# Optimization experiments

Hardware: AMD Instinct MI355X
Metric: run time of the kernel (lower is better)

Reference implementation:

```python
import jax, jax.numpy as jnp
import numpy as np

DIM = 1024; H = 16; KVH = 4; HD = 64          # head_dim = DIM // H
I = 2048                                       # intermediate_size = 2*DIM
N = 16                                         # ssm_state_size
DTR = 64                                       # dt_rank = DIM // 16
K = 4                                          # conv kernel
BASE = 10000.0
EPS = 1.1920929e-07                            # torch F.rms_norm default eps (fp32 finfo eps)

def rms_norm(x):
    return x * jax.lax.rsqrt(jnp.mean(x * x, axis=-1, keepdims=True) + EPS)

def rope_tables(S, dims):
    inv = 1.0 / BASE ** (jnp.arange(0, dims, 2, dtype=jnp.float32) / dims)
    f = jnp.outer(jnp.arange(S, dtype=jnp.float32), inv)   # [S, dims//2]
    return jnp.cos(f), jnp.sin(f)

def apply_rope(x, cos, sin):
    half = x.shape[-1] // 2
    x1, x2 = x[..., :half], x[..., half:]
    return jnp.concatenate([x1 * cos + x2 * sin, -x1 * sin + x2 * cos], axis=-1)

def setup_inputs() -> dict:
    key = jax.random.key(0)
    ks = jax.random.split(key, 12)
    B, S = 2, 2048
    def w(k, shape, s=0.02):
        return jax.random.normal(k, shape, jnp.float32) * s
    return {
        "x": jax.random.normal(ks[0], (B, S, DIM), jnp.float32),
        "W_mamba": w(ks[1], (2 * I, DIM)),
        "W_q": w(ks[2], (DIM, DIM)),
        "W_kv": w(ks[3], (2 * KVH * HD, DIM)),
        "q_gain": jnp.full((H,), 1.0, jnp.float32),
        "conv_w": w(ks[4], (I, K), 0.2),
        "conv_b": jnp.zeros((I,), jnp.float32),
        "W_xproj": w(ks[5], (DTR + 2 * N, I)),
        "W_dt": w(ks[6], (I, DTR)),
        "b_dt": w(ks[7], (I,), 0.5),
        "A_log": jnp.log(jnp.broadcast_to(jnp.arange(1, N + 1, dtype=jnp.float32), (I, N))),
        "D": jnp.ones((I,), jnp.float32),
        "W_mamba_out": w(ks[8], (DIM, I)),
        "W_proj": w(ks[9], (DIM, DIM)),
        "merge_alpha": jnp.zeros((1,), jnp.float32),
    }

def reference(x, W_mamba, W_q, W_kv, q_gain, conv_w, conv_b, W_xproj, W_dt, b_dt,
              A_log, D, W_mamba_out, W_proj, merge_alpha):
    B, S, _ = x.shape
    # --- parallel input projection for the mamba branch ---
    mp = x @ W_mamba.T                         # [B,S,2I]
    x_ssm, gate = mp[..., :I], mp[..., I:]
    # --- attention branch (GQA + full RoPE + per-head q gain) ---
    q = (x @ W_q.T).reshape(B, S, H, HD).transpose(0, 2, 1, 3)
    kv = x @ W_kv.T
    k = kv[..., :KVH * HD].reshape(B, S, KVH, HD).transpose(0, 2, 1, 3)
    v = kv[..., KVH * HD:].reshape(B, S, KVH, HD).transpose(0, 2, 1, 3)
    q = rms_norm(q); k = rms_norm(k)
    cos, sin = rope_tables(S, HD)
    q = apply_rope(q, cos, sin)
    k = apply_rope(k, cos, sin)
    q = q * q_gain[None, :, None, None]
    nrep = H // KVH
    k = jnp.repeat(k, nrep, axis=1)
    v = jnp.repeat(v, nrep, axis=1)
    scores = jnp.einsum('bhqd,bhkd->bhqk', q, k) / jnp.sqrt(jnp.float32(HD))
    mask = jnp.tril(jnp.ones((S, S), bool))
    scores = jnp.where(mask, scores, -jnp.inf)
    y = jnp.einsum('bhqk,bhkd->bhqd', jax.nn.softmax(scores, axis=-1), v)
    attn_out = y.transpose(0, 2, 1, 3).reshape(B, S, DIM)
    # --- mamba/SSM branch: causal depthwise conv1d + silu ---
    xc = x_ssm.transpose(0, 2, 1)              # [B,I,S]
    u = jax.lax.conv_general_dilated(xc, conv_w[:, None, :], (1,), [(K - 1, 0)],
                                     dimension_numbers=('NCH', 'OIH', 'NCH'),
                                     feature_group_count=I) + conv_b[None, :, None]
    u = u * jax.nn.sigmoid(u)                  # silu, [B,I,S]
    u_bsi = u.transpose(0, 2, 1)               # [B,S,I]
    params = u_bsi @ W_xproj.T                 # [B,S,DTR+2N]
    dt_low = params[..., :DTR]
    Bm = params[..., DTR:DTR + N]
    Cm = params[..., DTR + N:]
    delta = jax.nn.softplus(dt_low @ W_dt.T + b_dt)   # [B,S,I] (delta_bias + softplus)
    A = -jnp.exp(A_log)                        # [I,N]
    def step(state, inp):
        d_t, b_t, c_t, u_t = inp               # [B,I],[B,N],[B,N],[B,I]
        dA = jnp.exp(d_t[:, :, None] * A[None])
        state = state * dA + d_t[:, :, None] * b_t[:, None, :] * u_t[:, :, None]
        y_t = jnp.sum(state * c_t[:, None, :], axis=-1)
        return state, y_t
    xs = (delta.transpose(1, 0, 2), Bm.transpose(1, 0, 2),
          Cm.transpose(1, 0, 2), u_bsi.transpose(1, 0, 2))
    state0 = jnp.zeros((B, I, N), x.dtype)
    _, ys = jax.lax.scan(step, state0, xs)     # ys: [S,B,I]
    y_ssm = ys.transpose(1, 0, 2) + u_bsi * D  # + D skip
    y_ssm = y_ssm * (gate * jax.nn.sigmoid(gate))      # gated by silu(z)
    mamba_out = y_ssm @ W_mamba_out.T          # [B,S,DIM]
    # --- gated merge + output projection ---
    alpha = jax.nn.sigmoid(merge_alpha)
    merged = alpha * attn_out + (1.0 - alpha) * mamba_out
    return merged @ W_proj.T
```

## Files before the change

kernel.cpp:

```cpp
#include <hip/hip_runtime.h>
#include <hip/hip_bf16.h>

#define B_   2
#define S_   2048
#define T_   4096
#define DIM_ 1024
#define H_   16
#define KVH_ 4
#define HD_  64
#define I_   2048
#define N_   16
#define DTR_ 64
#define MB   ((size_t)1 << 20)

typedef __hip_bfloat16 bf16;
typedef __attribute__((ext_vector_type(8))) short short8;
typedef __attribute__((ext_vector_type(4))) short short4v;
typedef __attribute__((ext_vector_type(4))) float f32x4;

__device__ __forceinline__ float b2f(bf16 v){ return __bfloat162float(v); }
__device__ __forceinline__ bf16  f2b(float v){ return __float2bfloat16(v); }
__device__ __forceinline__ float s2f(short s){
  return __builtin_bit_cast(float, ((unsigned int)(unsigned short)s) << 16);
}
__device__ __forceinline__ short f2s(float v){
  return (short)__builtin_bit_cast(unsigned short, f2b(v));
}

__device__ __forceinline__ void async16(const void* g, void* l) {
  __builtin_amdgcn_global_load_lds((__attribute__((address_space(1))) void*)g,
                                   (__attribute__((address_space(3))) void*)l, 16, 0, 0);
}

__global__ __launch_bounds__(256)
void cast_f2b(const float* __restrict__ in, bf16* __restrict__ out, int n4)
{
  const int i = blockIdx.x * 256 + threadIdx.x;
  if (i >= n4) return;
  const float4 v = ((const float4*)in)[i];
  short4v o;
  o.x = f2s(v.x); o.y = f2s(v.y); o.z = f2s(v.z); o.w = f2s(v.w);
  *(short4v*)(out + (size_t)i * 4) = o;
}

template<int MODE, int TS>
__global__ __launch_bounds__(256)
void gemm_nt(const bf16* __restrict__ A, int lda,
             const bf16* __restrict__ W, int ldw,
             void* __restrict__ C, int ldc,
             bf16* __restrict__ Ct, int ldt,
             const float* __restrict__ bias,
             int M, int N, int K)
{
  __shared__ __align__(16) bf16 As[128*32];
  __shared__ __align__(16) bf16 Bs[128*32];
  const int tid  = threadIdx.x;
  const int lane = tid & 63;
  const int wave = tid >> 6;
  const int l16  = lane & 15;
  const int quad = lane >> 4;
  const int wm   = (wave >> 1) << 6;
  const int wn   = (wave & 1) << 6;
  const int m0   = blockIdx.x << 7;
  const int n0   = blockIdx.y << 7;

  f32x4 acc[4][4];
  const f32x4 zero = {0.f, 0.f, 0.f, 0.f};
  #pragma unroll
  for (int i = 0; i < 4; i++)
    #pragma unroll
    for (int j = 0; j < 4; j++) acc[i][j] = zero;

  for (int k0 = 0; k0 < K; k0 += 32) {
    #pragma unroll
    for (int p = 0; p < 2; p++) {
      const int linear = ((p << 8) + tid) << 4;
      const int row    = linear >> 6;
      const int inrow  = linear & 63;
      async16(A + (size_t)(m0 + row) * lda + k0 + (inrow >> 1), (char*)As + linear);
      int wr = n0 + row; if (wr > N - 1) wr = N - 1;
      async16(W + (size_t)wr * ldw + k0 + (inrow >> 1), (char*)Bs + linear);
    }
    __syncthreads();
    short8 af[4], bfr[4];
    #pragma unroll
    for (int mt = 0; mt < 4; mt++)
      af[mt] = *(const short8*)((const char*)As + ((wm + (mt << 4) + l16) << 6) + (quad << 4));
    #pragma unroll
    for (int nt = 0; nt < 4; nt++)
      bfr[nt] = *(const short8*)((const char*)Bs + ((wn + (nt << 4) + l16) << 6) + (quad << 4));
    #pragma unroll
    for (int mt = 0; mt < 4; mt++)
      #pragma unroll
      for (int nt = 0; nt < 4; nt++)
        acc[mt][nt] = __builtin_amdgcn_mfma_f32_16x16x32_bf16(af[mt], bfr[nt], acc[mt][nt], 0, 0, 0);
    __syncthreads();
  }

  #pragma unroll
  for (int mt = 0; mt < 4; mt++) {
    #pragma unroll
    for (int nt = 0; nt < 4; nt++) {
      const int col = n0 + wn + (nt << 4) + l16;
      if (col >= N) continue;
      const int rowbase = m0 + wm + (mt << 4) + (quad << 2);
      float v[4];
      #pragma unroll
      for (int r = 0; r < 4; r++) {
        float t = acc[mt][nt][r];
        if (MODE == 2) {
          t += bias[col];
          t = (t > 20.f) ? t : log1pf(__expf(t));
        }
        v[r] = t;
      }
      if (TS == 0 || TS == 2) {
        #pragma unroll
        for (int r = 0; r < 4; r++) {
          if (MODE == 0) ((float*)C)[(size_t)(rowbase + r) * ldc + col] = v[r];
          else           ((bf16*)C)[(size_t)(rowbase + r) * ldc + col] = f2b(v[r]);
        }
      }
      if (TS >= 1) {
        short4v p;
        #pragma unroll
        for (int r = 0; r < 4; r++) p[r] = f2s(v[r]);
        *(short4v*)(Ct + (size_t)col * ldt + rowbase) = p;
      }
    }
  }
}

__global__ __launch_bounds__(256)
void qkv_prep(const bf16* __restrict__ qraw, const bf16* __restrict__ kvraw,
              const float* __restrict__ q_gain,
              bf16* __restrict__ qn, bf16* __restrict__ kn, bf16* __restrict__ vt)
{
  const int wid  = blockIdx.x * 4 + (threadIdx.x >> 6);
  const int lane = threadIdx.x & 63;
  const int t    = wid / 24;
  const int slot = wid % 24;
  const int b = t >> 11, s = t & 2047;

  float val;
  if (slot < 16)       val = b2f(qraw [(size_t)t * 1024 + slot * 64 + lane]);
  else if (slot < 20)  val = b2f(kvraw[(size_t)t * 512  + (slot - 16) * 64 + lane]);
  else                 val = b2f(kvraw[(size_t)t * 512  + 256 + (slot - 20) * 64 + lane]);

  if (slot < 20) {
    float ss = val * val;
    #pragma unroll
    for (int off = 32; off; off >>= 1) ss += __shfl_xor(ss, off);
    val *= rsqrtf(ss * (1.0f / 64.0f) + 1.1920929e-07f);
    const int j = lane & 31;
    const float x1 = __shfl(val, j);
    const float x2 = __shfl(val, j + 32);
    const float inv = powf(10000.0f, -(float)j * (1.0f / 32.0f));
    const float ang = (float)s * inv;
    const float c = cosf(ang), sn = sinf(ang);
    val = (lane < 32) ? (x1 * c + x2 * sn) : (x2 * c - x1 * sn);
  }
  if (slot < 16) {
    val *= q_gain[slot];
    qn[((size_t)(b * 16 + slot) * 2048 + s) * 64 + lane] = f2b(val);
  } else if (slot < 20) {
    kn[((size_t)(b * 4 + (slot - 16)) * 2048 + s) * 64 + lane] = f2b(val);
  } else {
    vt[((size_t)(b * 4 + (slot - 20)) * 64 + lane) * 2048 + s] = f2b(val);
  }
}

__global__ __launch_bounds__(256)
void attn_fwd(const bf16* __restrict__ qn, const bf16* __restrict__ kn,
              const bf16* __restrict__ vt, bf16* __restrict__ attn)
{
  __shared__ __align__(16) bf16 Plds[4][16][32];
  const int b = blockIdx.z, h = blockIdx.y, q0 = blockIdx.x * 64;
  const int wave = threadIdx.x >> 6, lane = threadIdx.x & 63;
  const int l16 = lane & 15, quad = lane >> 4;
  const int kvh = h >> 2;
  const bf16* Q  = qn + (size_t)(b * 16 + h)   * 2048 * 64;
  const bf16* Kp = kn + (size_t)(b * 4 + kvh)  * 2048 * 64;
  const bf16* Vt = vt + (size_t)(b * 4 + kvh)  * 64 * 2048;

  const int qrow_l = q0 + wave * 16 + l16;
  const short8 qf0 = *(const short8*)(Q + (size_t)qrow_l * 64 + quad * 8);
  const short8 qf1 = *(const short8*)(Q + (size_t)qrow_l * 64 + 32 + quad * 8);

  f32x4 acc[4];
  const f32x4 zero = {0.f, 0.f, 0.f, 0.f};
  #pragma unroll
  for (int i = 0; i < 4; i++) acc[i] = zero;
  float m_r[4], l_r[4];
  #pragma unroll
  for (int r = 0; r < 4; r++) { m_r[r] = -1e30f; l_r[r] = 0.f; }

  const int nkt = (q0 + 64) >> 5;
  for (int kt = 0; kt < nkt; kt++) {
    const int kb = kt << 5;
    const short8 kfA0 = *(const short8*)(Kp + (size_t)(kb + l16) * 64 + quad * 8);
    const short8 kfA1 = *(const short8*)(Kp + (size_t)(kb + l16) * 64 + 32 + quad * 8);
    const short8 kfB0 = *(const short8*)(Kp + (size_t)(kb + 16 + l16) * 64 + quad * 8);
    const short8 kfB1 = *(const short8*)(Kp + (size_t)(kb + 16 + l16) * 64 + 32 + quad * 8);
    f32x4 sA = zero, sB = zero;
    sA = __builtin_amdgcn_mfma_f32_16x16x32_bf16(qf0, kfA0, sA, 0, 0, 0);
    sA = __builtin_amdgcn_mfma_f32_16x16x32_bf16(qf1, kfA1, sA, 0, 0, 0);
    sB = __builtin_amdgcn_mfma_f32_16x16x32_bf16(qf0, kfB0, sB, 0, 0, 0);
    sB = __builtin_amdgcn_mfma_f32_16x16x32_bf16(qf1, kfB1, sB, 0, 0, 0);

    const int colA = kb + l16, colB = kb + 16 + l16;
    float pA[4], pB[4], alpha[4];
    #pragma unroll
    for (int r = 0; r < 4; r++) {
      const int row = q0 + wave * 16 + quad * 4 + r;
      float a  = sA[r] * 0.125f;
      float bb = sB[r] * 0.125f;
      if (colA > row) a  = -1e30f;
      if (colB > row) bb = -1e30f;
      float tm = fmaxf(a, bb);
      #pragma unroll
      for (int off = 8; off; off >>= 1) tm = fmaxf(tm, __shfl_xor(tm, off));
      const float nm = fmaxf(m_r[r], tm);
      alpha[r] = __expf(m_r[r] - nm);
      m_r[r] = nm;
      const float pa = __expf(a - nm), pb = __expf(bb - nm);
      pA[r] = pa; pB[r] = pb;
      float ps = pa + pb;
      #pragma unroll
      for (int off = 8; off; off >>= 1) ps += __shfl_xor(ps, off);
      l_r[r] = l_r[r] * alpha[r] + ps;
    }
    #pragma unroll
    for (int nt = 0; nt < 4; nt++)
      #pragma unroll
      for (int r = 0; r < 4; r++) acc[nt][r] *= alpha[r];

    __syncthreads();
    #pragma unroll
    for (int r = 0; r < 4; r++) {
      Plds[wave][quad * 4 + r][l16]      = f2b(pA[r]);
      Plds[wave][quad * 4 + r][16 + l16] = f2b(pB[r]);
    }
    __syncthreads();
    const short8 pf = *(const short8*)(&Plds[wave][l16][quad * 8]);
    #pragma unroll
    for (int nt = 0; nt < 4; nt++) {
      const short8 vf = *(const short8*)(Vt + (size_t)(nt * 16 + l16) * 2048 + kb + quad * 8);
      acc[nt] = __builtin_amdgcn_mfma_f32_16x16x32_bf16(pf, vf, acc[nt], 0, 0, 0);
    }
  }

  #pragma unroll
  for (int nt = 0; nt < 4; nt++)
    #pragma unroll
    for (int r = 0; r < 4; r++) {
      const int row = q0 + wave * 16 + quad * 4 + r;
      attn[((size_t)b * 2048 + row) * 1024 + h * 64 + nt * 16 + l16] = f2b(acc[nt][r] / l_r[r]);
    }
}

__global__ __launch_bounds__(256)
void conv_silu_t(const bf16* __restrict__ xssmT, const float* __restrict__ cw,
                 const float* __restrict__ cb, bf16* __restrict__ uT)
{
  const int i = blockIdx.x;
  const int t = blockIdx.y * 256 + threadIdx.x;
  const int s = t & 2047;
  float acc = cb[i];
  #pragma unroll
  for (int kk = 0; kk < 4; kk++) {
    if (s - 3 + kk >= 0)
      acc += s2f(__builtin_bit_cast(short, xssmT[(size_t)i * 4096 + t - 3 + kk])) * cw[i * 4 + kk];
  }
  const float sig = 1.f / (1.f + __expf(-acc));
  uT[(size_t)i * 4096 + t] = f2b(acc * sig);
}

__global__ __launch_bounds__(256)
void transpose_bf16(const bf16* __restrict__ in, bf16* __restrict__ out,
                    int R, int C)
{
  __shared__ bf16 tile[64][65];
  const int c0 = blockIdx.x * 64, r0 = blockIdx.y * 64;
  #pragma unroll
  for (int it = 0; it < 2; it++) {
    const int linear = (it * 256 + threadIdx.x) * 8;
    const int r = linear >> 6, cc = linear & 63;
    const short8 v = *(const short8*)(in + (size_t)(r0 + r) * C + c0 + cc);
    #pragma unroll
    for (int k = 0; k < 8; k++)
      tile[r][cc + k] = __builtin_bit_cast(bf16, (unsigned short)v[k]);
  }
  __syncthreads();
  #pragma unroll
  for (int it = 0; it < 2; it++) {
    const int linear = (it * 256 + threadIdx.x) * 8;
    const int oc = linear >> 6, k = linear & 63;
    short8 v;
    #pragma unroll
    for (int kk = 0; kk < 8; kk++)
      v[kk] = (short)__builtin_bit_cast(unsigned short, tile[k + kk][oc]);
    *(short8*)(out + (size_t)(c0 + oc) * R + r0 + k) = v;
  }
}

__global__ __launch_bounds__(256)
void finish_y(const bf16* __restrict__ yT, const bf16* __restrict__ gT,
              bf16* __restrict__ out)
{
  __shared__ bf16 tile[64][65];
  const int t0 = blockIdx.x * 64, i0 = blockIdx.y * 64;
  #pragma unroll
  for (int it = 0; it < 2; it++) {
    const int linear = (it * 256 + threadIdx.x) * 8;
    const int r = linear >> 6, cc = linear & 63;
    const size_t off = (size_t)(i0 + r) * 4096 + t0 + cc;
    const short8 y8 = *(const short8*)(yT + off);
    const short8 g8 = *(const short8*)(gT + off);
    #pragma unroll
    for (int k = 0; k < 8; k++) {
      const float g  = s2f(g8[k]);
      const float gs = g / (1.f + __expf(-g));
      tile[r][cc + k] = f2b(s2f(y8[k]) * gs);
    }
  }
  __syncthreads();
  #pragma unroll
  for (int it = 0; it < 2; it++) {
    const int linear = (it * 256 + threadIdx.x) * 8;
    const int oc = linear >> 6, k = linear & 63;
    short8 v;
    #pragma unroll
    for (int kk = 0; kk < 8; kk++)
      v[kk] = (short)__builtin_bit_cast(unsigned short, tile[k + kk][oc]);
    *(short8*)(out + (size_t)(t0 + oc) * 2048 + i0 + k) = v;
  }
}

__global__ __launch_bounds__(256)
void ssm_scan(const bf16* __restrict__ dltT, const bf16* __restrict__ uT,
              const bf16* __restrict__ prmT, const float* __restrict__ A_log,
              const float* __restrict__ Dv, bf16* __restrict__ youtT)
{
  __shared__ float Pl[16][17], Fl[16][17], Il[16][17];
  const int blk = blockIdx.x;
  const int b = blk >> 11, i = blk & 2047;
  const int n = threadIdx.x & 15, c = threadIdx.x >> 4;
  const float a  = -__expf(A_log[i * 16 + n]);
  const float Di = Dv[i];
  const size_t rowoff = (size_t)b * 2048 + c * 128;
  const bf16* dp = dltT  + (size_t)i * 4096 + rowoff;
  const bf16* up = uT    + (size_t)i * 4096 + rowoff;
  const bf16* Bp = prmT  + (size_t)(64 + n) * 4096 + rowoff;
  const bf16* Cp = prmT  + (size_t)(80 + n) * 4096 + rowoff;
  bf16*       yp = youtT + (size_t)i * 4096 + rowoff;

  float P = 1.f, F = 0.f;
  for (int j0 = 0; j0 < 128; j0 += 8) {
    const short8 d8 = *(const short8*)(dp + j0);
    const short8 u8 = *(const short8*)(up + j0);
    const short8 B8 = *(const short8*)(Bp + j0);
    #pragma unroll
    for (int j = 0; j < 8; j++) {
      const float dt = s2f(d8[j]);
      const float dA = __expf(dt * a);
      P *= dA;
      F = F * dA + dt * s2f(u8[j]) * s2f(B8[j]);
    }
  }
  Pl[n][c] = P; Fl[n][c] = F;
  __syncthreads();

  if (threadIdx.x < 16) {
    const int nn = threadIdx.x;
    float s = 0.f;
    #pragma unroll
    for (int cc = 0; cc < 16; cc++) {
      Il[nn][cc] = s;
      s = Fl[nn][cc] + Pl[nn][cc] * s;
    }
  }
  __syncthreads();

  float state = Il[n][c];
  for (int j0 = 0; j0 < 128; j0 += 8) {
    const short8 d8 = *(const short8*)(dp + j0);
    const short8 u8 = *(const short8*)(up + j0);
    const short8 B8 = *(const short8*)(Bp + j0);
    const short8 C8 = *(const short8*)(Cp + j0);
    short8 o8;
    #pragma unroll
    for (int j = 0; j < 8; j++) {
      const float dt = s2f(d8[j]);
      const float ut = s2f(u8[j]);
      const float dA = __expf(dt * a);
      state = state * dA + dt * ut * s2f(B8[j]);
      float y = state * s2f(C8[j]);
      y += __shfl_xor(y, 1); y += __shfl_xor(y, 2);
      y += __shfl_xor(y, 4); y += __shfl_xor(y, 8);
      o8[j] = f2s(y + ut * Di);
    }
    if (n == 0) *(short8*)(yp + j0) = o8;
  }
}

__global__ __launch_bounds__(256)
void merge_k(const bf16* __restrict__ attn, const bf16* __restrict__ mamba,
             const float* __restrict__ malpha, bf16* __restrict__ merged)
{
  const size_t idx = (size_t)blockIdx.x * 256 + threadIdx.x;
  const float al = 1.f / (1.f + __expf(-malpha[0]));
  merged[idx] = f2b(al * b2f(attn[idx]) + (1.f - al) * b2f(mamba[idx]));
}

extern "C" void kernel_launch(void* const* d_in, const int* in_sizes, int n_in,
                              void* d_out, int out_size, void* d_ws, size_t ws_size,
                              hipStream_t stream)
{
  const float* x_f     = (const float*)d_in[0];
  const float* Wm_f    = (const float*)d_in[1];
  const float* Wq_f    = (const float*)d_in[2];
  const float* Wkv_f   = (const float*)d_in[3];
  const float* q_gain  = (const float*)d_in[4];
  const float* conv_w  = (const float*)d_in[5];
  const float* conv_b  = (const float*)d_in[6];
  const float* Wxp_f   = (const float*)d_in[7];
  const float* Wdt_f   = (const float*)d_in[8];
  const float* b_dt    = (const float*)d_in[9];
  const float* A_log   = (const float*)d_in[10];
  const float* Dv      = (const float*)d_in[11];
  const float* Wmo_f   = (const float*)d_in[12];
  const float* Wp_f    = (const float*)d_in[13];
  const float* malpha  = (const float*)d_in[14];

  char* wp = (char*)d_ws;
  bf16*  xb    = (bf16*)(wp + 0 * MB);
  bf16*  Wm_b  = (bf16*)(wp + 8 * MB);
  bf16*  Wq_b  = (bf16*)(wp + 16 * MB);
  bf16*  Wkv_b = (bf16*)(wp + 18 * MB);
  bf16*  xssmT = (bf16*)(wp + 19 * MB);
  bf16*  gateT = (bf16*)(wp + 35 * MB);
  bf16*  u     = (bf16*)(wp + 51 * MB);
  bf16*  uT    = (bf16*)(wp + 67 * MB);
  bf16*  qraw  = (bf16*)(wp + 83 * MB);
  bf16*  kvraw = (bf16*)(wp + 91 * MB);
  bf16*  dltT  = (bf16*)(wp + 95 * MB);
  bf16*  qn    = (bf16*)(wp + 0 * MB);
  bf16*  kn    = (bf16*)(wp + 8 * MB);
  bf16*  vtb   = (bf16*)(wp + 10 * MB);
  bf16*  Wxp_b = (bf16*)(wp + 12 * MB);
  bf16*  Wdt_b = (bf16*)(wp + 12 * MB + 512 * 1024);
  bf16*  prm   = (bf16*)(wp + 13 * MB);
  bf16*  prmT  = (bf16*)(wp + 13 * MB + 768 * 1024);
  bf16*  Wp_b  = (bf16*)(wp + 16 * MB);
  bf16*  attnb = (bf16*)(wp + 83 * MB);
  bf16*  Wmo_b = (bf16*)(wp + 91 * MB);
  bf16*  ybuf  = (bf16*)(wp + 19 * MB);
  bf16*  ybufT = (bf16*)(wp + 51 * MB);
  bf16*  mam   = (bf16*)(wp + 35 * MB);
  bf16*  mrg   = (bf16*)(wp + 43 * MB);
  (void)ws_size; (void)in_sizes; (void)n_in; (void)out_size;

  auto cast = [&](const float* src, bf16* dst, int n) {
    const int n4 = n >> 2;
    cast_f2b<<<dim3((n4 + 255) / 256), 256, 0, stream>>>(src, dst, n4);
  };
  cast(x_f,   xb,    T_ * 1024);
  cast(Wm_f,  Wm_b,  4096 * 1024);
  cast(Wq_f,  Wq_b,  1024 * 1024);
  cast(Wkv_f, Wkv_b, 512 * 1024);

  gemm_nt<1,1><<<dim3(32, 16), 256, 0, stream>>>(xb, 1024, Wm_b,               1024, nullptr, 0, xssmT, 4096, nullptr, T_, 2048, 1024);
  gemm_nt<1,1><<<dim3(32, 16), 256, 0, stream>>>(xb, 1024, Wm_b + 2048 * 1024, 1024, nullptr, 0, gateT, 4096, nullptr, T_, 2048, 1024);
  gemm_nt<1,0><<<dim3(32, 8),  256, 0, stream>>>(xb, 1024, Wq_b,  1024, qraw,  1024, nullptr, 0, nullptr, T_, 1024, 1024);
  gemm_nt<1,0><<<dim3(32, 4),  256, 0, stream>>>(xb, 1024, Wkv_b, 1024, kvraw,  512, nullptr, 0, nullptr, T_,  512, 1024);

  qkv_prep<<<dim3((T_ * 24) / 4), 256, 0, stream>>>(qraw, kvraw, q_gain, qn, kn, vtb);
  conv_silu_t<<<dim3(2048, 16), 256, 0, stream>>>(xssmT, conv_w, conv_b, uT);
  attn_fwd<<<dim3(32, 16, 2), 256, 0, stream>>>(qn, kn, vtb, attnb);
  transpose_bf16<<<dim3(64, 32), 256, 0, stream>>>(uT, u, 2048, 4096);

  cast(Wxp_f, Wxp_b, 96 * 2048);
  cast(Wdt_f, Wdt_b, 2048 * 64);
  cast(Wmo_f, Wmo_b, 1024 * 2048);
  cast(Wp_f,  Wp_b,  1024 * 1024);

  gemm_nt<1,2><<<dim3(32, 1),  256, 0, stream>>>(u, 2048, Wxp_b, 2048, prm, 96, prmT, 4096, nullptr, T_, 96, 2048);
  gemm_nt<2,1><<<dim3(32, 16), 256, 0, stream>>>(prm, 96, Wdt_b, 64, nullptr, 0, dltT, 4096, b_dt, T_, 2048, 64);
  ssm_scan<<<dim3(4096), 256, 0, stream>>>(dltT, uT, prmT, A_log, Dv, ybufT);
  finish_y<<<dim3(64, 32), 256, 0, stream>>>(ybufT, gateT, ybuf);
  gemm_nt<1,0><<<dim3(32, 8),  256, 0, stream>>>(ybuf, 2048, Wmo_b, 2048, mam, 1024, nullptr, 0, nullptr, T_, 1024, 2048);

  merge_k<<<dim3(16384), 256, 0, stream>>>(attnb, mam, malpha, mrg);
  gemm_nt<0,0><<<dim3(32, 8),  256, 0, stream>>>(mrg, 1024, Wp_b, 1024, (float*)d_out, 1024, nullptr, 0, nullptr, T_, 1024, 1024);
}
```

Measured before the change: 903.9 us.

## Widen attention key tile, bound loop per wave, drop block barriers

The causal attention loop now processes 64 keys per iteration instead of 32, and each wave stops at its own 16-row causal bound rather than the whole block's bound. The two __syncthreads around the per-wave P staging buffer are removed, since each wave only touches its own LDS slice. That slice is padded to a stride of 80 to reduce bank conflicts. The aim is to cut barrier stalls, loop overhead and wasted masked work, at the cost of more registers for the wider score tile.

```diff
diff --git a/kernel.cpp b/kernel.cpp
--- a/kernel.cpp
+++ b/kernel.cpp
@@ -174,18 +174,18 @@
 void attn_fwd(const bf16* __restrict__ qn, const bf16* __restrict__ kn,
               const bf16* __restrict__ vt, bf16* __restrict__ attn)
 {
-  __shared__ __align__(16) bf16 Plds[4][16][32];
-  const int b = blockIdx.z, h = blockIdx.y, q0 = blockIdx.x * 64;
+  __shared__ __align__(16) bf16 Plds[4][16][80];
+  const int b = blockIdx.z, h = blockIdx.y;
   const int wave = threadIdx.x >> 6, lane = threadIdx.x & 63;
   const int l16 = lane & 15, quad = lane >> 4;
+  const int q0 = blockIdx.x * 64 + wave * 16;
   const int kvh = h >> 2;
-  const bf16* Q  = qn + (size_t)(b * 16 + h)   * 2048 * 64;
-  const bf16* Kp = kn + (size_t)(b * 4 + kvh)  * 2048 * 64;
-  const bf16* Vt = vt + (size_t)(b * 4 + kvh)  * 64 * 2048;
-
-  const int qrow_l = q0 + wave * 16 + l16;
-  const short8 qf0 = *(const short8*)(Q + (size_t)qrow_l * 64 + quad * 8);
-  const short8 qf1 = *(const short8*)(Q + (size_t)qrow_l * 64 + 32 + quad * 8);
+  const bf16* Q  = qn + (size_t)(b * 16 + h)  * 2048 * 64;
+  const bf16* Kp = kn + (size_t)(b * 4 + kvh) * 2048 * 64;
+  const bf16* Vt = vt + (size_t)(b * 4 + kvh) * 64 * 2048;
+
+  const short8 qf0 = *(const short8*)(Q + (size_t)(q0 + l16) * 64 + quad * 8);
+  const short8 qf1 = *(const short8*)(Q + (size_t)(q0 + l16) * 64 + 32 + quad * 8);
 
   f32x4 acc[4];
   const f32x4 zero = {0.f, 0.f, 0.f, 0.f};
@@ -195,39 +195,41 @@
   #pragma unroll
   for (int r = 0; r < 4; r++) { m_r[r] = -1e30f; l_r[r] = 0.f; }
 
-  const int nkt = (q0 + 64) >> 5;
-  for (int kt = 0; kt < nkt; kt++) {
-    const int kb = kt << 5;
-    const short8 kfA0 = *(const short8*)(Kp + (size_t)(kb + l16) * 64 + quad * 8);
-    const short8 kfA1 = *(const short8*)(Kp + (size_t)(kb + l16) * 64 + 32 + quad * 8);
-    const short8 kfB0 = *(const short8*)(Kp + (size_t)(kb + 16 + l16) * 64 + quad * 8);
-    const short8 kfB1 = *(const short8*)(Kp + (size_t)(kb + 16 + l16) * 64 + 32 + quad * 8);
-    f32x4 sA = zero, sB = zero;
-    sA = __builtin_amdgcn_mfma_f32_16x16x32_bf16(qf0, kfA0, sA, 0, 0, 0);
-    sA = __builtin_amdgcn_mfma_f32_16x16x32_bf16(qf1, kfA1, sA, 0, 0, 0);
-    sB = __builtin_amdgcn_mfma_f32_16x16x32_bf16(qf0, kfB0, sB, 0, 0, 0);
-    sB = __builtin_amdgcn_mfma_f32_16x16x32_bf16(qf1, kfB1, sB, 0, 0, 0);
-
-    const int colA = kb + l16, colB = kb + 16 + l16;
-    float pA[4], pB[4], alpha[4];
+  const int kend = q0 + 16;
+  for (int kb = 0; kb < kend; kb += 64) {
+    f32x4 s[4];
+    #pragma unroll
+    for (int t = 0; t < 4; t++) {
+      const bf16* kr = Kp + (size_t)(kb + t * 16 + l16) * 64;
+      const short8 kf0 = *(const short8*)(kr + quad * 8);
+      const short8 kf1 = *(const short8*)(kr + 32 + quad * 8);
+      f32x4 sv = zero;
+      sv = __builtin_amdgcn_mfma_f32_16x16x32_bf16(qf0, kf0, sv, 0, 0, 0);
+      sv = __builtin_amdgcn_mfma_f32_16x16x32_bf16(qf1, kf1, sv, 0, 0, 0);
+      s[t] = sv;
+    }
+    float alpha[4], p[4][4];
     #pragma unroll
     for (int r = 0; r < 4; r++) {
-      const int row = q0 + wave * 16 + quad * 4 + r;
-      float a  = sA[r] * 0.125f;
-      float bb = sB[r] * 0.125f;
-      if (colA > row) a  = -1e30f;
-      if (colB > row) bb = -1e30f;
-      float tm = fmaxf(a, bb);
-      #pragma unroll
-      for (int off = 8; off; off >>= 1) tm = fmaxf(tm, __shfl_xor(tm, off));
+      const int row = q0 + quad * 4 + r;
+      float v[4];
+      #pragma unroll
+      for (int t = 0; t < 4; t++) {
+        float x = s[t][r] * 0.125f;
+        if (kb + t * 16 + l16 > row) x = -1e30f;
+        v[t] = x;
+      }
+      float tm = fmaxf(fmaxf(v[0], v[1]), fmaxf(v[2], v[3]));
+      tm = fmaxf(tm, __shfl_xor(tm, 1)); tm = fmaxf(tm, __shfl_xor(tm, 2));
+      tm = fmaxf(tm, __shfl_xor(tm, 4)); tm = fmaxf(tm, __shfl_xor(tm, 8));
       const float nm = fmaxf(m_r[r], tm);
       alpha[r] = __expf(m_r[r] - nm);
       m_r[r] = nm;
-      const float pa = __expf(a - nm), pb = __expf(bb - nm);
-      pA[r] = pa; pB[r] = pb;
-      float ps = pa + pb;
-      #pragma unroll
-      for (int off = 8; off; off >>= 1) ps += __shfl_xor(ps, off);
+      float ps = 0.f;
+      #pragma unroll
+      for (int t = 0; t < 4; t++) { p[r][t] = __expf(v[t] - nm); ps += p[r][t]; }
+      ps += __shfl_xor(ps, 1); ps += __shfl_xor(ps, 2);
+      ps += __shfl_xor(ps, 4); ps += __shfl_xor(ps, 8);
       l_r[r] = l_r[r] * alpha[r] + ps;
     }
     #pragma unroll
@@ -235,26 +237,28 @@
       #pragma unroll
       for (int r = 0; r < 4; r++) acc[nt][r] *= alpha[r];
 
-    __syncthreads();
+    #pragma unroll
+    for (int r = 0; r < 4; r++)
+      #pragma unroll
+      for (int t = 0; t < 4; t++)
+        Plds[wave][quad * 4 + r][t * 16 + l16] = f2b(p[r][t]);
+
+    #pragma unroll
+    for (int c = 0; c < 2; c++) {
+      const short8 pf = *(const short8*)(&Plds[wave][l16][c * 32 + quad * 8]);
+      #pragma unroll
+      for (int nt = 0; nt < 4; nt++) {
+        const short8 vf = *(const short8*)(Vt + (size_t)(nt * 16 + l16) * 2048 + kb + c * 32 + quad * 8);
+        acc[nt] = __builtin_amdgcn_mfma_f32_16x16x32_bf16(pf, vf, acc[nt], 0, 0, 0);
+      }
+    }
+  }
+
+  #pragma unroll
+  for (int nt = 0; nt < 4; nt++)
     #pragma unroll
     for (int r = 0; r < 4; r++) {
-      Plds[wave][quad * 4 + r][l16]      = f2b(pA[r]);
-      Plds[wave][quad * 4 + r][16 + l16] = f2b(pB[r]);
-    }
-    __syncthreads();
-    const short8 pf = *(const short8*)(&Plds[wave][l16][quad * 8]);
-    #pragma unroll
-    for (int nt = 0; nt < 4; nt++) {
-      const short8 vf = *(const short8*)(Vt + (size_t)(nt * 16 + l16) * 2048 + kb + quad * 8);
-      acc[nt] = __builtin_amdgcn_mfma_f32_16x16x32_bf16(pf, vf, acc[nt], 0, 0, 0);
-    }
-  }
-
-  #pragma unroll
-  for (int nt = 0; nt < 4; nt++)
-    #pragma unroll
-    for (int r = 0; r < 4; r++) {
-      const int row = q0 + wave * 16 + quad * 4 + r;
+      const int row = q0 + quad * 4 + r;
       attn[((size_t)b * 2048 + row) * 1024 + h * 64 + nt * 16 + l16] = f2b(acc[nt][r] / l_r[r]);
     }
 }
```

Result: no change. 898.7 us (-0.6%).
